# Kernel optimization log

Measured on AMD Instinct MI355X. Metric: run time of the kernel, lower is better.

Reference implementation:

```python
import jax, jax.numpy as jnp
import numpy as np

CUT_SIZE = 224  # cut_size init arg
CUTN = 32       # cutn init arg
CUT_POW = 1.0


def setup_inputs() -> dict:
    key = jax.random.key(0)
    B, C, H, W = 16, 3, 512, 512
    x = jax.random.normal(key, (B, C, H, W), dtype=jnp.float32)
    # Replicate the module's host-side RNG: size = rand()**cut_pow*(max-min)+min,
    # offset = randint(0, side - size + 1). Generated with numpy for determinism.
    rs = np.random.RandomState(0)
    max_size = min(H, W)
    min_size = min(H, W, CUT_SIZE)
    sizes = (rs.rand(CUTN) ** CUT_POW * (max_size - min_size) + min_size).astype(np.int32)
    offsetx = np.floor(rs.rand(CUTN) * (W - sizes + 1)).astype(np.int32)
    offsety = np.floor(rs.rand(CUTN) * (H - sizes + 1)).astype(np.int32)
    return {
        "x": x,
        "sizes": jnp.asarray(sizes),
        "offsetx": jnp.asarray(offsetx),
        "offsety": jnp.asarray(offsety),
    }


def reference(x, sizes, offsetx, offsety):
    # x: [B, C, H, W]; sizes/offsetx/offsety: [cutn] int32
    B, C, H, W = x.shape
    i = jnp.arange(CUT_SIZE, dtype=jnp.int32)
    # PyTorch F.interpolate default 'nearest': src = floor(out_idx * in/out)
    yidx = offsety[:, None] + (i[None, :] * sizes[:, None]) // CUT_SIZE  # [cutn, cut]
    xidx = offsetx[:, None] + (i[None, :] * sizes[:, None]) // CUT_SIZE  # [cutn, cut]
    # Fused crop + nearest-resize for all cutouts via one batched gather
    out = x[:, :, yidx[:, :, None], xidx[:, None, :]]  # [B, C, cutn, cut, cut]
    out = jnp.transpose(out, (2, 0, 1, 3, 4))           # [cutn, B, C, cut, cut]
    return out.reshape(CUTN * B, C, CUT_SIZE, CUT_SIZE)  # matches th.cat over cutn
```

## Files before the change

kernel.cpp:

```cpp
#include <hip/hip_runtime.h>


#define CUT_SIZE 224
#define CUTN     32
#define BATCH    16
#define CHAN     3
#define HEIGHT   512
#define WIDTH    512
#define GROUPS   (CUTN * BATCH * CHAN)
#define I_PER_WAVE 56
#define CHUNKS   (CUT_SIZE / I_PER_WAVE)
#define WPB      4
#define DEPTH    3

typedef const __attribute__((address_space(1))) void* gas_ptr;
typedef __attribute__((address_space(3))) void*       las_ptr;

__device__ __forceinline__ void stage_row(const float* src_row, float* lds_buf, int lane)
{
    __builtin_amdgcn_global_load_lds((gas_ptr)(src_row + lane * 4),
                                     (las_ptr)(lds_buf), 16, 0, 0);
    __builtin_amdgcn_global_load_lds((gas_ptr)(src_row + 256 + lane * 4),
                                     (las_ptr)(lds_buf + 256), 16, 0, 0);
}

__global__ __launch_bounds__(256) void make_cutouts_kernel(
    const float* __restrict__ x,
    const int*   __restrict__ sizes,
    const int*   __restrict__ offsetx,
    const int*   __restrict__ offsety,
    float*       __restrict__ out)
{
    __shared__ __align__(16) float lds[WPB][DEPTH][WIDTH];

    const int wid  = threadIdx.x >> 6;
    const int lane = threadIdx.x & 63;

    const int task  = blockIdx.x * WPB + wid;
    const int g     = task >> 2;
    const int chunk = task & 3;

    const int c  = g % CHAN;
    const int tb = g / CHAN;
    const int b  = tb % BATCH;
    const int n  = tb / BATCH;

    const int sz = sizes[n];
    const int ox = offsetx[n];
    const int oy = offsety[n];

    const float* img  = x + (size_t)(b * CHAN + c) * (HEIGHT * WIDTH);
    float*       outg = out + (size_t)g * (CUT_SIZE * CUT_SIZE)
                            + (size_t)(chunk * I_PER_WAVE) * CUT_SIZE;

    const unsigned usz = (unsigned)sz;
    const int xi0 = ox + (int)(((unsigned)(lane      ) * usz) / CUT_SIZE);
    const int xi1 = ox + (int)(((unsigned)(lane +  64) * usz) / CUT_SIZE);
    const int xi2 = ox + (int)(((unsigned)(lane + 128) * usz) / CUT_SIZE);
    const int xi3 = (lane < 32)
                  ? ox + (int)(((unsigned)(lane + 192) * usz) / CUT_SIZE)
                  : xi0;

    float* p0 = &lds[wid][0][0];
    float* p1 = &lds[wid][1][0];
    float* p2 = &lds[wid][2][0];

    const int ibase = chunk * I_PER_WAVE;

    #define ROW_PTR(K) (img + (size_t)(oy + (int)(((unsigned)((ibase + (K)) * sz)) / CUT_SIZE)) * WIDTH)

    stage_row(ROW_PTR(0), p0, lane);
    stage_row(ROW_PTR(1), p1, lane);
    stage_row(ROW_PTR(2), p2, lane);

    for (int k = 0; k < I_PER_WAVE; ++k) {
        if      (k <  I_PER_WAVE - 2) { asm volatile("s_waitcnt vmcnt(4)" ::: "memory"); }
        else if (k == I_PER_WAVE - 2) { asm volatile("s_waitcnt vmcnt(2)" ::: "memory"); }
        else                          { asm volatile("s_waitcnt vmcnt(0)" ::: "memory"); }
        __builtin_amdgcn_sched_barrier(0);

        const float v0 = p0[xi0];
        const float v1 = p0[xi1];
        const float v2 = p0[xi2];
        const float v3 = p0[xi3];

        asm volatile("s_waitcnt lgkmcnt(0)" ::: "memory");
        __builtin_amdgcn_sched_barrier(0);

        if (k + DEPTH < I_PER_WAVE) {
            stage_row(ROW_PTR(k + DEPTH), p0, lane);
        }

        float* orow = outg + (size_t)k * CUT_SIZE;
        orow[lane      ] = v0;
        orow[lane +  64] = v1;
        orow[lane + 128] = v2;
        if (lane < 32) orow[lane + 192] = v3;

        float* t = p0; p0 = p1; p1 = p2; p2 = t;
    }
    #undef ROW_PTR
}

extern "C" void kernel_launch(void* const* d_in, const int* in_sizes, int n_in,
                              void* d_out, int out_size, void* d_ws, size_t ws_size,
                              hipStream_t stream) {
    const float* x       = (const float*)d_in[0];
    const int*   sizes   = (const int*)d_in[1];
    const int*   offsetx = (const int*)d_in[2];
    const int*   offsety = (const int*)d_in[3];
    float*       out     = (float*)d_out;

    const int grid = GROUPS * CHUNKS / WPB;
    make_cutouts_kernel<<<grid, 256, 0, stream>>>(x, sizes, offsetx, offsety, out);
}
```

Measured before the change: 394.3 us.

## Invert loop to read each input row slice once and scatter to all cutouts

```diff
diff --git a/kernel.cpp b/kernel.cpp
--- a/kernel.cpp
+++ b/kernel.cpp
@@ -7,11 +7,10 @@
 #define CHAN     3
 #define HEIGHT   512
 #define WIDTH    512
-#define GROUPS   (CUTN * BATCH * CHAN)
-#define I_PER_WAVE 56
-#define CHUNKS   (CUT_SIZE / I_PER_WAVE)
+#define R_SLICE  16
+#define NSLICE   (HEIGHT / R_SLICE)
+#define NIMG     (BATCH * CHAN)
 #define WPB      4
-#define DEPTH    3
 
 typedef const __attribute__((address_space(1))) void* gas_ptr;
 typedef __attribute__((address_space(3))) void*       las_ptr;
@@ -31,75 +30,67 @@
     const int*   __restrict__ offsety,
     float*       __restrict__ out)
 {
-    __shared__ __align__(16) float lds[WPB][DEPTH][WIDTH];
+    __shared__ __align__(16) float lds[R_SLICE][WIDTH];
 
     const int wid  = threadIdx.x >> 6;
     const int lane = threadIdx.x & 63;
 
-    const int task  = blockIdx.x * WPB + wid;
-    const int g     = task >> 2;
-    const int chunk = task & 3;
+    const int bid   = blockIdx.x;
+    const int img   = bid >> 5;
+    const int slice = bid & (NSLICE - 1);
+    const int b     = img / CHAN;
+    const int c     = img % CHAN;
+    const int y0    = slice * R_SLICE;
 
-    const int c  = g % CHAN;
-    const int tb = g / CHAN;
-    const int b  = tb % BATCH;
-    const int n  = tb / BATCH;
+    const float* img_p = x + (size_t)img * (HEIGHT * WIDTH);
 
-    const int sz = sizes[n];
-    const int ox = offsetx[n];
-    const int oy = offsety[n];
+    #pragma unroll
+    for (int r = 0; r < R_SLICE / WPB; ++r) {
+        const int row = wid * (R_SLICE / WPB) + r;
+        stage_row(img_p + (size_t)(y0 + row) * WIDTH, &lds[row][0], lane);
+    }
+    asm volatile("s_waitcnt vmcnt(0)" ::: "memory");
+    __syncthreads();
 
-    const float* img  = x + (size_t)(b * CHAN + c) * (HEIGHT * WIDTH);
-    float*       outg = out + (size_t)g * (CUT_SIZE * CUT_SIZE)
-                            + (size_t)(chunk * I_PER_WAVE) * CUT_SIZE;
+    for (int nn = 0; nn < CUTN / WPB; ++nn) {
+        const int n  = wid + nn * WPB;
+        const int sz = sizes[n];
+        const int ox = offsetx[n];
+        const int oy = offsety[n];
 
-    const unsigned usz = (unsigned)sz;
-    const int xi0 = ox + (int)(((unsigned)(lane      ) * usz) / CUT_SIZE);
-    const int xi1 = ox + (int)(((unsigned)(lane +  64) * usz) / CUT_SIZE);
-    const int xi2 = ox + (int)(((unsigned)(lane + 128) * usz) / CUT_SIZE);
-    const int xi3 = (lane < 32)
-                  ? ox + (int)(((unsigned)(lane + 192) * usz) / CUT_SIZE)
-                  : xi0;
+        const int d0 = y0 - oy;
+        const int d1 = y0 + R_SLICE - oy;
+        int i0 = (d0 <= 0) ? 0 : (int)(((unsigned)(d0 * CUT_SIZE) + (unsigned)sz - 1u) / (unsigned)sz);
+        int i1 = (d1 <= 0) ? 0 : (int)(((unsigned)(d1 * CUT_SIZE) + (unsigned)sz - 1u) / (unsigned)sz);
+        if (i1 > CUT_SIZE) i1 = CUT_SIZE;
+        if (i0 >= i1) continue;
 
-    float* p0 = &lds[wid][0][0];
-    float* p1 = &lds[wid][1][0];
-    float* p2 = &lds[wid][2][0];
+        const unsigned usz = (unsigned)sz;
+        const int xi0 = ox + (int)(((unsigned)(lane      ) * usz) / CUT_SIZE);
+        const int xi1 = ox + (int)(((unsigned)(lane +  64) * usz) / CUT_SIZE);
+        const int xi2 = ox + (int)(((unsigned)(lane + 128) * usz) / CUT_SIZE);
+        const int xi3 = (lane < 32)
+                      ? ox + (int)(((unsigned)(lane + 192) * usz) / CUT_SIZE)
+                      : xi0;
 
-    const int ibase = chunk * I_PER_WAVE;
+        float* og = out + (size_t)((n * BATCH + b) * CHAN + c) * (CUT_SIZE * CUT_SIZE);
 
-    #define ROW_PTR(K) (img + (size_t)(oy + (int)(((unsigned)((ibase + (K)) * sz)) / CUT_SIZE)) * WIDTH)
+        for (int i = i0; i < i1; ++i) {
+            const int y = oy + (int)(((unsigned)(i * (int)usz)) / CUT_SIZE);
+            const float* lrow = &lds[y - y0][0];
 
-    stage_row(ROW_PTR(0), p0, lane);
-    stage_row(ROW_PTR(1), p1, lane);
-    stage_row(ROW_PTR(2), p2, lane);
+            const float v0 = lrow[xi0];
+            const float v1 = lrow[xi1];
+            const float v2 = lrow[xi2];
+            const float v3 = lrow[xi3];
 
-    for (int k = 0; k < I_PER_WAVE; ++k) {
-        if      (k <  I_PER_WAVE - 2) { asm volatile("s_waitcnt vmcnt(4)" ::: "memory"); }
-        else if (k == I_PER_WAVE - 2) { asm volatile("s_waitcnt vmcnt(2)" ::: "memory"); }
-        else                          { asm volatile("s_waitcnt vmcnt(0)" ::: "memory"); }
-        __builtin_amdgcn_sched_barrier(0);
-
-        const float v0 = p0[xi0];
-        const float v1 = p0[xi1];
-        const float v2 = p0[xi2];
-        const float v3 = p0[xi3];
-
-        asm volatile("s_waitcnt lgkmcnt(0)" ::: "memory");
-        __builtin_amdgcn_sched_barrier(0);
-
-        if (k + DEPTH < I_PER_WAVE) {
-            stage_row(ROW_PTR(k + DEPTH), p0, lane);
+            float* orow = og + (size_t)i * CUT_SIZE;
+            orow[lane      ] = v0;
+            orow[lane +  64] = v1;
+            orow[lane + 128] = v2;
+            if (lane < 32) orow[lane + 192] = v3;
         }
-
-        float* orow = outg + (size_t)k * CUT_SIZE;
-        orow[lane      ] = v0;
-        orow[lane +  64] = v1;
-        orow[lane + 128] = v2;
-        if (lane < 32) orow[lane + 192] = v3;
-
-        float* t = p0; p0 = p1; p1 = p2; p2 = t;
     }
-    #undef ROW_PTR
 }
 
 extern "C" void kernel_launch(void* const* d_in, const int* in_sizes, int n_in,
@@ -111,6 +102,6 @@
     const int*   offsety = (const int*)d_in[3];
     float*       out     = (float*)d_out;
 
-    const int grid = GROUPS * CHUNKS / WPB;
+    const int grid = NIMG * NSLICE;
     make_cutouts_kernel<<<grid, 256, 0, stream>>>(x, sizes, offsetx, offsety, out);
 }
```

Measured after the change: 352.5 us. -10.6%, faster.
